# Optimization experiments

Hardware: AMD Instinct MI355X
Metric: run time of the kernel (lower is better)

The kernel has to match this reference:

```python
import jax, jax.numpy as jnp
import numpy as np
import math

VOCAB = 32000
D = 256
MAX_SEQ = 128
B, S = 32, 128
EPS = 1e-5


def cexp(p):
    # exp(1j*p) for real p, staying in complex64 under default x32
    return jax.lax.complex(jnp.cos(p), jnp.sin(p))


def setup_inputs() -> dict:
    key = jax.random.key(0)
    ks = jax.random.split(key, 10)
    x = jax.random.randint(ks[0], (B, S), 0, VOCAB)
    emb = jax.random.normal(ks[1], (VOCAB, D), dtype=jnp.float32)
    q_rot = jax.random.uniform(ks[2], (D,), minval=-math.pi, maxval=math.pi)
    k_rot = jax.random.uniform(ks[3], (D,), minval=-math.pi, maxval=math.pi)
    v_rot = jax.random.uniform(ks[4], (D,), minval=-math.pi, maxval=math.pi)
    # orthogonal init for ff_real via QR
    a = jax.random.normal(ks[5], (D, D), dtype=jnp.float32)
    q, r = jnp.linalg.qr(a)
    ff_real = q * jnp.sign(jnp.diag(r))[None, :]
    ff_imag = jax.random.uniform(ks[6], (D, D), minval=-0.01, maxval=0.01)
    wr = jax.random.normal(ks[7], (VOCAB, D), dtype=jnp.float32) / math.sqrt(D)
    br = jnp.zeros((VOCAB,), dtype=jnp.float32)
    wi = jax.random.normal(ks[8], (VOCAB, D), dtype=jnp.float32) / math.sqrt(D)
    bi = jnp.zeros((VOCAB,), dtype=jnp.float32)
    return {"x": x, "emb": emb, "q_rot": q_rot, "k_rot": k_rot, "v_rot": v_rot,
            "ff_real": ff_real, "ff_imag": ff_imag, "wr": wr, "br": br, "wi": wi, "bi": bi}


def _pos_phase(seq_len):
    pos = jnp.arange(MAX_SEQ, dtype=jnp.float32)[:, None]
    dim = jnp.arange(D, dtype=jnp.float32)[None, :]
    freq = 1.0 / (10000.0 ** (dim / D))
    return (pos * freq * math.pi)[:seq_len]  # [S, D]


def complex_norm(state):
    mag = jnp.abs(state)                                  # [B,S,D]
    mean_mag = mag.mean(axis=-1, keepdims=True)
    std_mag = jnp.std(mag, axis=-1, keepdims=True, ddof=1)  # torch default unbiased
    norm_mag = (mag - mean_mag) / (std_mag + EPS)
    scale = jnp.tanh(norm_mag) / (mag + EPS)
    return state * scale.astype(jnp.complex64)


def reference(x, emb, q_rot, k_rot, v_rot, ff_real, ff_imag, wr, br, wi, bi):
    seq_len = x.shape[1]
    mag = jnp.tanh(emb[x])                                # [B,S,D] float32
    state = mag.astype(jnp.complex64) * cexp(_pos_phase(seq_len))[None]  # [B,S,D] c64
    q = state * cexp(q_rot)
    k = state * cexp(k_rot)
    v = state * cexp(v_rot)
    interference = jnp.einsum('bsd,btd->bst', q, jnp.conj(k))
    attn_logits = interference.real / math.sqrt(D)        # [B,S,S]
    causal = jnp.tril(jnp.ones((seq_len, seq_len), dtype=bool))
    attn_logits = jnp.where(causal[None], attn_logits, -jnp.inf)
    attn_w = jax.nn.softmax(attn_logits * 8.0, axis=-1)   # [B,S,S]
    attn_out = jnp.einsum('bst,btd->bsd', attn_w.astype(jnp.complex64), v)
    state = state + attn_out
    ff = jax.lax.complex(ff_real, ff_imag)
    state = state @ ff                                    # [B,S,D]
    state = complex_norm(state)
    logits = state.real @ wr.T + br + state.imag @ wi.T + bi  # [B,S,V]
    return logits
```

## Files before the change

### kernel.cpp

```cpp
#include <hip/hip_runtime.h>

#define DD   256
#define SEQ  128
#define NB   32
#define VOC  32000
#define ROWS (NB * SEQ)
#define KK   512

typedef __attribute__((ext_vector_type(8))) short short8;
typedef __attribute__((ext_vector_type(4))) float f32x4;

__device__ inline unsigned short f2bf(float f) {
  unsigned int u = __float_as_uint(f);
  u += 0x7FFF + ((u >> 16) & 1);
  return (unsigned short)(u >> 16);
}

__device__ inline void gload16(const void* g, void* l) {
  __builtin_amdgcn_global_load_lds(
      (const __attribute__((address_space(1))) void*)g,
      (__attribute__((address_space(3))) void*)l, 16, 0, 0);
}

__global__ __launch_bounds__(256) void k_prep(
    const float* __restrict__ wr, const float* __restrict__ wi,
    const float* __restrict__ br, const float* __restrict__ bi,
    const float* __restrict__ qrot, const float* __restrict__ krot,
    const float* __restrict__ vrot,
    unsigned short* __restrict__ Wb, float* __restrict__ bias,
    float* __restrict__ rotcs) {
  int idx = blockIdx.x * 256 + threadIdx.x;
  int v = idx >> 7, c = idx & 127;
  const float* src = (c < 64) ? (wr + (size_t)v * DD + c * 4)
                              : (wi + (size_t)v * DD + (c - 64) * 4);
  float4 f = *(const float4*)src;
  ushort4 o;
  o.x = f2bf(f.x); o.y = f2bf(f.y); o.z = f2bf(f.z); o.w = f2bf(f.w);
  *(ushort4*)(Wb + (size_t)v * KK + c * 4) = o;
  if (c == 0) bias[v] = br[v] + bi[v];
  if (idx < DD) {
    float s0, c0;
    sincosf(qrot[idx], &s0, &c0); rotcs[idx] = c0;          rotcs[DD + idx] = s0;
    sincosf(krot[idx], &s0, &c0); rotcs[2 * DD + idx] = c0; rotcs[3 * DD + idx] = s0;
    sincosf(vrot[idx], &s0, &c0); rotcs[4 * DD + idx] = c0; rotcs[5 * DD + idx] = s0;
  }
}

__global__ __launch_bounds__(256) void k_embed(
    const int* __restrict__ x, const float* __restrict__ emb,
    const float* __restrict__ rotcs,
    float* __restrict__ Sb, float* __restrict__ Qb,
    float* __restrict__ Kb, float* __restrict__ Vb) {
  int row = blockIdx.x;
  int s = row & (SEQ - 1);
  int d = threadIdx.x;
  int tok = x[row];
  float m = tanhf(emb[(size_t)tok * DD + d]);
  float freq = __expf(-(float)d * (9.210340371976184f / 256.f));
  float p = (float)s * freq * 3.14159265358979f;
  float sp, cp;
  __sincosf(p, &sp, &cp);
  size_t base = (size_t)row * KK + d;
  Sb[base] = m * cp; Sb[base + DD] = m * sp;
  float cr, sr;
  cr = rotcs[d];          sr = rotcs[DD + d];
  Qb[base] = m * (cp * cr - sp * sr); Qb[base + DD] = m * (sp * cr + cp * sr);
  cr = rotcs[2 * DD + d]; sr = rotcs[3 * DD + d];
  Kb[base] = m * (cp * cr - sp * sr); Kb[base + DD] = m * (sp * cr + cp * sr);
  cr = rotcs[4 * DD + d]; sr = rotcs[5 * DD + d];
  Vb[base] = m * (cp * cr - sp * sr); Vb[base + DD] = m * (sp * cr + cp * sr);
}

#define QBLK 16
#define QPAD (KK + 4)
__global__ __launch_bounds__(512) void k_attn(
    const float* __restrict__ Qb, const float* __restrict__ Kb,
    const float* __restrict__ Vb, const float* __restrict__ Sb,
    float* __restrict__ S2) {
  int blk = blockIdx.x;
  int b = blk >> 3, g = blk & 7;
  int tid = threadIdx.x;
  int q = tid >> 5, t5 = tid & 31;
  int tt = t5 & 15, half = t5 >> 4;
  __shared__ __align__(16) float Ql[QBLK][QPAD];
  __shared__ __align__(16) float KVl[QBLK][QPAD];
  __shared__ float w[QBLK][SEQ];
  size_t qrow0 = (size_t)b * SEQ + g * QBLK;
  const float* qsrc = Qb + qrow0 * KK;
#pragma unroll
  for (int i = 0; i < 4; ++i) {
    int idx = i * 512 + tid;
    int r = idx >> 7, c = idx & 127;
    *(float4*)&Ql[r][c * 4] = *(const float4*)&qsrc[(size_t)r * KK + c * 4];
  }
  int ntile = g + 1;
  int srow = g * QBLK + q;
  for (int kt = 0; kt < ntile; ++kt) {
    __syncthreads();
    const float* ksrc = Kb + ((size_t)b * SEQ + kt * QBLK) * KK;
#pragma unroll
    for (int i = 0; i < 4; ++i) {
      int idx = i * 512 + tid;
      int r = idx >> 7, c = idx & 127;
      *(float4*)&KVl[r][c * 4] = *(const float4*)&ksrc[(size_t)r * KK + c * 4];
    }
    __syncthreads();
    const float4* qrow = (const float4*)&Ql[q][half * 256];
    const float4* krow = (const float4*)&KVl[tt][half * 256];
    float a0 = 0.f, a1 = 0.f, a2 = 0.f, a3 = 0.f;
#pragma unroll 8
    for (int cc = 0; cc < 64; ++cc) {
      float4 qa = qrow[cc], ka = krow[cc];
      a0 += qa.x * ka.x; a1 += qa.y * ka.y; a2 += qa.z * ka.z; a3 += qa.w * ka.w;
    }
    float acc = (a0 + a1) + (a2 + a3);
    acc += __shfl_xor(acc, 16);
    int t = kt * QBLK + tt;
    if (half == 0) w[q][t] = (t <= srow) ? acc * 0.5f : -INFINITY;
  }
  __syncthreads();
  int nk = ntile * QBLK;
  float mx = -INFINITY;
  for (int t = tt; t < nk; t += 16) mx = fmaxf(mx, w[q][t]);
#pragma unroll
  for (int o = 8; o; o >>= 1) mx = fmaxf(mx, __shfl_xor(mx, o));
  float sm = 0.f;
  for (int t = tt; t < nk; t += 16) {
    float e = __expf(w[q][t] - mx);
    if (half == 0) w[q][t] = e;
    sm += e;
  }
#pragma unroll
  for (int o = 8; o; o >>= 1) sm += __shfl_xor(sm, o);
  float inv = 1.f / sm;
  float4 facc[4] = {};
  for (int kt = 0; kt < ntile; ++kt) {
    __syncthreads();
    const float* vsrc = Vb + ((size_t)b * SEQ + kt * QBLK) * KK;
#pragma unroll
    for (int i = 0; i < 4; ++i) {
      int idx = i * 512 + tid;
      int r = idx >> 7, c = idx & 127;
      *(float4*)&KVl[r][c * 4] = *(const float4*)&vsrc[(size_t)r * KK + c * 4];
    }
    __syncthreads();
#pragma unroll
    for (int t1 = 0; t1 < QBLK; ++t1) {
      float wv = w[q][kt * QBLK + t1];
#pragma unroll
      for (int j = 0; j < 4; ++j) {
        float4 v4 = *(const float4*)&KVl[t1][tt * 4 + (j + 4 * half) * 64];
        facc[j].x += wv * v4.x; facc[j].y += wv * v4.y;
        facc[j].z += wv * v4.z; facc[j].w += wv * v4.w;
      }
    }
  }
  const float* ssrc = Sb + (qrow0 + q) * KK;
  float* dst = S2 + (qrow0 + q) * KK;
#pragma unroll
  for (int j = 0; j < 4; ++j) {
    int d0 = tt * 4 + (j + 4 * half) * 64;
    float4 sv = *(const float4*)&ssrc[d0];
    float4 o;
    o.x = sv.x + facc[j].x * inv; o.y = sv.y + facc[j].y * inv;
    o.z = sv.z + facc[j].z * inv; o.w = sv.w + facc[j].w * inv;
    *(float4*)&dst[d0] = o;
  }
}

__global__ __launch_bounds__(256) void k_ffnorm(
    const float* __restrict__ S2, const float* __restrict__ ffr,
    const float* __restrict__ ffi, unsigned short* __restrict__ X) {
  int row0 = blockIdx.x * 8;
  int d = threadIdx.x;
  __shared__ __align__(16) float in[8][KK];
  __shared__ float mg[8][DD];
  __shared__ float stats[16];
#pragma unroll
  for (int i = 0; i < 4; ++i) {
    int idx = i * 256 + d;
    *(float4*)&((float*)in)[idx * 4] = *(const float4*)&S2[(size_t)row0 * KK + idx * 4];
  }
  __syncthreads();
  float nr[8] = {0,0,0,0,0,0,0,0}, ni[8] = {0,0,0,0,0,0,0,0};
  for (int e4 = 0; e4 < 64; ++e4) {
    int e = e4 * 4;
    float fr0 = ffr[(e+0)*DD + d], fr1 = ffr[(e+1)*DD + d];
    float fr2 = ffr[(e+2)*DD + d], fr3 = ffr[(e+3)*DD + d];
    float fi0 = ffi[(e+0)*DD + d], fi1 = ffi[(e+1)*DD + d];
    float fi2 = ffi[(e+2)*DD + d], fi3 = ffi[(e+3)*DD + d];
#pragma unroll
    for (int r = 0; r < 8; ++r) {
      float4 av = *(const float4*)&in[r][e];
      float4 cv = *(const float4*)&in[r][DD + e];
      nr[r] += av.x*fr0 - cv.x*fi0 + av.y*fr1 - cv.y*fi1
             + av.z*fr2 - cv.z*fi2 + av.w*fr3 - cv.w*fi3;
      ni[r] += av.x*fi0 + cv.x*fr0 + av.y*fi1 + cv.y*fr1
             + av.z*fi2 + cv.z*fr2 + av.w*fi3 + cv.w*fr3;
    }
  }
#pragma unroll
  for (int r = 0; r < 8; ++r) mg[r][d] = sqrtf(nr[r]*nr[r] + ni[r]*ni[r]);
  __syncthreads();
  int wv = d >> 6, ln = d & 63;
#pragma unroll
  for (int k = 0; k < 2; ++k) {
    int r = wv + k * 4;
    float s0 = mg[r][ln] + mg[r][ln+64] + mg[r][ln+128] + mg[r][ln+192];
#pragma unroll
    for (int o = 32; o; o >>= 1) s0 += __shfl_xor(s0, o);
    float mean = s0 * (1.f / 256.f);
    float var = 0.f;
#pragma unroll
    for (int j = 0; j < 4; ++j) { float t2 = mg[r][ln + j*64] - mean; var += t2*t2; }
#pragma unroll
    for (int o = 32; o; o >>= 1) var += __shfl_xor(var, o);
    if (ln == 0) { stats[r*2] = mean; stats[r*2+1] = sqrtf(var * (1.f/255.f)); }
  }
  __syncthreads();
#pragma unroll
  for (int r = 0; r < 8; ++r) {
    float mean2 = stats[r*2], stdv = stats[r*2+1];
    float mag = mg[r][d];
    float norm = (mag - mean2) / (stdv + 1e-5f);
    float sc = tanhf(norm) / (mag + 1e-5f);
    size_t base = (size_t)(row0 + r) * KK + d;
    X[base] = f2bf(nr[r] * sc);
    X[base + DD] = f2bf(ni[r] * sc);
  }
}

__global__ __launch_bounds__(256, 3) void k_gemm(
    const unsigned short* __restrict__ X, const unsigned short* __restrict__ Wb,
    const float* __restrict__ bias, float* __restrict__ out) {
  __shared__ __align__(16) unsigned short At[128 * 64];
  __shared__ __align__(16) unsigned short Bt[128 * 64];
  int tid = threadIdx.x;
  int lane = tid & 63, wave = tid >> 6;
  int wr = wave >> 1, wc = wave & 1;
  int orig = blockIdx.x;
  int wg = (orig & 7) * 1000 + (orig >> 3);
  int mt = wg & 31, nt = wg >> 5;
  size_t rowA0 = (size_t)mt * 128;
  size_t rowB0 = (size_t)nt * 128;

  int srow = lane >> 3;
  int schunk = ((lane & 7) ^ (srow & 7)) * 8;

  f32x4 acc[4][4] = {};
  int l15 = lane & 15, hi = lane >> 4;

  for (int kt = 0; kt < 8; ++kt) {
    if (kt) { asm volatile("" ::: "memory"); __builtin_amdgcn_s_barrier(); }
    const int k0 = kt * 64;
#pragma unroll
    for (int j = 0; j < 4; ++j) {
      int rbase = wave * 32 + j * 8;
      gload16(&X [(rowA0 + rbase + srow) * KK + k0 + schunk], &At[rbase * 64]);
      gload16(&Wb[(rowB0 + rbase + srow) * KK + k0 + schunk], &Bt[rbase * 64]);
    }
    asm volatile("s_waitcnt vmcnt(0)" ::: "memory");
    __builtin_amdgcn_s_barrier();
    asm volatile("" ::: "memory");
#pragma unroll
    for (int ks = 0; ks < 2; ++ks) {
      int cXor = (ks * 4 + hi) ^ (l15 & 7);
      short8 a[4], bb[4];
#pragma unroll
      for (int ni = 0; ni < 4; ++ni)
        bb[ni] = *(const short8*)&Bt[(wc * 64 + ni * 16 + l15) * 64 + cXor * 8];
#pragma unroll
      for (int mi = 0; mi < 4; ++mi)
        a[mi] = *(const short8*)&At[(wr * 64 + mi * 16 + l15) * 64 + cXor * 8];
#pragma unroll
      for (int mi = 0; mi < 4; ++mi)
#pragma unroll
        for (int ni = 0; ni < 4; ++ni)
          acc[mi][ni] = __builtin_amdgcn_mfma_f32_16x16x32_bf16(a[mi], bb[ni], acc[mi][ni], 0, 0, 0);
    }
  }

  int cr = lane >> 4, cc = lane & 15;
#pragma unroll
  for (int ni = 0; ni < 4; ++ni) {
    size_t col = rowB0 + wc * 64 + ni * 16 + cc;
    float bv = bias[col];
#pragma unroll
    for (int mi = 0; mi < 4; ++mi) {
#pragma unroll
      for (int j = 0; j < 4; ++j) {
        size_t rowc = rowA0 + wr * 64 + mi * 16 + cr * 4 + j;
        __builtin_nontemporal_store(acc[mi][ni][j] + bv, &out[rowc * VOC + col]);
      }
    }
  }
}

extern "C" void kernel_launch(void* const* d_in, const int* in_sizes, int n_in,
                              void* d_out, int out_size, void* d_ws, size_t ws_size,
                              hipStream_t stream) {
  const int* x      = (const int*)d_in[0];
  const float* emb  = (const float*)d_in[1];
  const float* qrot = (const float*)d_in[2];
  const float* krot = (const float*)d_in[3];
  const float* vrot = (const float*)d_in[4];
  const float* ffr  = (const float*)d_in[5];
  const float* ffi  = (const float*)d_in[6];
  const float* wr   = (const float*)d_in[7];
  const float* br   = (const float*)d_in[8];
  const float* wi   = (const float*)d_in[9];
  const float* bi   = (const float*)d_in[10];
  float* out = (float*)d_out;
  char* ws = (char*)d_ws;

  unsigned short* Wb = (unsigned short*)ws;
  float* bias = (float*)(ws + 32768000);
  float* Sb = (float*)(ws + 32896000);
  float* Qb = Sb + (size_t)ROWS * KK;
  float* Kb = Qb + (size_t)ROWS * KK;
  float* Vb = Kb + (size_t)ROWS * KK;
  float* S2 = Vb + (size_t)ROWS * KK;
  unsigned short* Xb = (unsigned short*)(S2 + (size_t)ROWS * KK);
  float* rotcs = S2;

  k_prep<<<dim3(VOC * 128 / 256), dim3(256), 0, stream>>>(wr, wi, br, bi, qrot, krot, vrot, Wb, bias, rotcs);
  k_embed<<<dim3(ROWS), dim3(256), 0, stream>>>(x, emb, rotcs, Sb, Qb, Kb, Vb);
  k_attn<<<dim3(NB * 8), dim3(512), 0, stream>>>(Qb, Kb, Vb, Sb, S2);
  k_ffnorm<<<dim3(ROWS / 8), dim3(256), 0, stream>>>(S2, ffr, ffi, Xb);
  k_gemm<<<dim3(8000), dim3(256), 0, stream>>>(Xb, Wb, bias, out);
}
```

Measured before the change: 330.8 us.

## Double-buffer LDS tiles in the output GEMM to overlap loads with MFMA

The GEMM kernel now uses two LDS buffers for the A and B tiles. It prefetches the next K-slice through global_load_lds while MFMAs run on the current slice, with one barrier per iteration instead of a wait-then-barrier before compute. This aims to hide global-load latency behind compute. In exchange, LDS use doubles and the launch-bounds occupancy hint drops from 3 to 2 blocks per CU. That can reduce latency hiding across blocks in a kernel that is largely bound by output stores.

New measurement: 357.3 us. 8.0% more time.

```diff
diff --git a/kernel.cpp b/kernel.cpp
--- a/kernel.cpp
+++ b/kernel.cpp
@@ -230,11 +230,11 @@
   }
 }
 
-__global__ __launch_bounds__(256, 3) void k_gemm(
+__global__ __launch_bounds__(256, 2) void k_gemm(
     const unsigned short* __restrict__ X, const unsigned short* __restrict__ Wb,
     const float* __restrict__ bias, float* __restrict__ out) {
-  __shared__ __align__(16) unsigned short At[128 * 64];
-  __shared__ __align__(16) unsigned short Bt[128 * 64];
+  __shared__ __align__(16) unsigned short At[2][128 * 64];
+  __shared__ __align__(16) unsigned short Bt[2][128 * 64];
   int tid = threadIdx.x;
   int lane = tid & 63, wave = tid >> 6;
   int wr = wave >> 1, wc = wave & 1;
@@ -250,35 +250,41 @@
   f32x4 acc[4][4] = {};
   int l15 = lane & 15, hi = lane >> 4;
 
+#define STAGE(t, b)                                                         \
+  { const int k0 = (t) * 64;                                                \
+    _Pragma("unroll")                                                       \
+    for (int j = 0; j < 4; ++j) {                                           \
+      int rbase = wave * 32 + j * 8;                                        \
+      gload16(&X [(rowA0 + rbase + srow) * KK + k0 + schunk],               \
+              &At[b][rbase * 64]);                                          \
+      gload16(&Wb[(rowB0 + rbase + srow) * KK + k0 + schunk],               \
+              &Bt[b][rbase * 64]); } }
+
+  STAGE(0, 0);
+  __syncthreads();
+
   for (int kt = 0; kt < 8; ++kt) {
-    if (kt) { asm volatile("" ::: "memory"); __builtin_amdgcn_s_barrier(); }
-    const int k0 = kt * 64;
-#pragma unroll
-    for (int j = 0; j < 4; ++j) {
-      int rbase = wave * 32 + j * 8;
-      gload16(&X [(rowA0 + rbase + srow) * KK + k0 + schunk], &At[rbase * 64]);
-      gload16(&Wb[(rowB0 + rbase + srow) * KK + k0 + schunk], &Bt[rbase * 64]);
-    }
-    asm volatile("s_waitcnt vmcnt(0)" ::: "memory");
-    __builtin_amdgcn_s_barrier();
-    asm volatile("" ::: "memory");
+    int buf = kt & 1;
+    if (kt < 7) STAGE(kt + 1, buf ^ 1);
 #pragma unroll
     for (int ks = 0; ks < 2; ++ks) {
       int cXor = (ks * 4 + hi) ^ (l15 & 7);
       short8 a[4], bb[4];
 #pragma unroll
       for (int ni = 0; ni < 4; ++ni)
-        bb[ni] = *(const short8*)&Bt[(wc * 64 + ni * 16 + l15) * 64 + cXor * 8];
+        bb[ni] = *(const short8*)&Bt[buf][(wc * 64 + ni * 16 + l15) * 64 + cXor * 8];
 #pragma unroll
       for (int mi = 0; mi < 4; ++mi)
-        a[mi] = *(const short8*)&At[(wr * 64 + mi * 16 + l15) * 64 + cXor * 8];
+        a[mi] = *(const short8*)&At[buf][(wr * 64 + mi * 16 + l15) * 64 + cXor * 8];
 #pragma unroll
       for (int mi = 0; mi < 4; ++mi)
 #pragma unroll
         for (int ni = 0; ni < 4; ++ni)
           acc[mi][ni] = __builtin_amdgcn_mfma_f32_16x16x32_bf16(a[mi], bb[ni], acc[mi][ni], 0, 0, 0);
     }
-  }
+    __syncthreads();
+  }
+#undef STAGE
 
   int cr = lane >> 4, cc = lane & 15;
 #pragma unroll
```

## Fold weight bf16 conversion into attention launch and compute rotations inline

Applied to the files above, without the earlier changes.

Removes the separate prep kernel. The weight-to-bf16 conversion and bias sum now run as extra blocks appended to the attention kernel grid, so that bandwidth-bound work can overlap with the small 256-block attention launch. The q/k/v rotation sin/cos values are computed per thread inside the embed kernel instead of being read from a precomputed table. The output GEMM also switches from nontemporal stores to plain stores. Trade-offs: each conversion block now asks for the attention kernel's LDS and 512-thread resources, embed threads do redundant sincosf work, and plain stores may pollute the cache.

Result: slower. 376.2 us (+13.7%).

```diff
diff --git a/kernel.cpp b/kernel.cpp
--- a/kernel.cpp
+++ b/kernel.cpp
@@ -22,33 +22,10 @@
       (__attribute__((address_space(3))) void*)l, 16, 0, 0);
 }
 
-__global__ __launch_bounds__(256) void k_prep(
-    const float* __restrict__ wr, const float* __restrict__ wi,
-    const float* __restrict__ br, const float* __restrict__ bi,
+__global__ __launch_bounds__(256) void k_embed(
+    const int* __restrict__ x, const float* __restrict__ emb,
     const float* __restrict__ qrot, const float* __restrict__ krot,
     const float* __restrict__ vrot,
-    unsigned short* __restrict__ Wb, float* __restrict__ bias,
-    float* __restrict__ rotcs) {
-  int idx = blockIdx.x * 256 + threadIdx.x;
-  int v = idx >> 7, c = idx & 127;
-  const float* src = (c < 64) ? (wr + (size_t)v * DD + c * 4)
-                              : (wi + (size_t)v * DD + (c - 64) * 4);
-  float4 f = *(const float4*)src;
-  ushort4 o;
-  o.x = f2bf(f.x); o.y = f2bf(f.y); o.z = f2bf(f.z); o.w = f2bf(f.w);
-  *(ushort4*)(Wb + (size_t)v * KK + c * 4) = o;
-  if (c == 0) bias[v] = br[v] + bi[v];
-  if (idx < DD) {
-    float s0, c0;
-    sincosf(qrot[idx], &s0, &c0); rotcs[idx] = c0;          rotcs[DD + idx] = s0;
-    sincosf(krot[idx], &s0, &c0); rotcs[2 * DD + idx] = c0; rotcs[3 * DD + idx] = s0;
-    sincosf(vrot[idx], &s0, &c0); rotcs[4 * DD + idx] = c0; rotcs[5 * DD + idx] = s0;
-  }
-}
-
-__global__ __launch_bounds__(256) void k_embed(
-    const int* __restrict__ x, const float* __restrict__ emb,
-    const float* __restrict__ rotcs,
     float* __restrict__ Sb, float* __restrict__ Qb,
     float* __restrict__ Kb, float* __restrict__ Vb) {
   int row = blockIdx.x;
@@ -63,23 +40,38 @@
   size_t base = (size_t)row * KK + d;
   Sb[base] = m * cp; Sb[base + DD] = m * sp;
   float cr, sr;
-  cr = rotcs[d];          sr = rotcs[DD + d];
+  sincosf(qrot[d], &sr, &cr);
   Qb[base] = m * (cp * cr - sp * sr); Qb[base + DD] = m * (sp * cr + cp * sr);
-  cr = rotcs[2 * DD + d]; sr = rotcs[3 * DD + d];
+  sincosf(krot[d], &sr, &cr);
   Kb[base] = m * (cp * cr - sp * sr); Kb[base + DD] = m * (sp * cr + cp * sr);
-  cr = rotcs[4 * DD + d]; sr = rotcs[5 * DD + d];
+  sincosf(vrot[d], &sr, &cr);
   Vb[base] = m * (cp * cr - sp * sr); Vb[base + DD] = m * (sp * cr + cp * sr);
 }
 
 #define QBLK 16
 #define QPAD (KK + 4)
-__global__ __launch_bounds__(512) void k_attn(
+__global__ __launch_bounds__(512) void k_attn_prep(
     const float* __restrict__ Qb, const float* __restrict__ Kb,
     const float* __restrict__ Vb, const float* __restrict__ Sb,
-    float* __restrict__ S2) {
+    float* __restrict__ S2,
+    const float* __restrict__ wr, const float* __restrict__ wi,
+    const float* __restrict__ br, const float* __restrict__ bi,
+    unsigned short* __restrict__ Wb, float* __restrict__ bias) {
+  int tid = threadIdx.x;
+  if (blockIdx.x >= 256) {
+    int idx = (blockIdx.x - 256) * 512 + tid;
+    int v = idx >> 7, c = idx & 127;
+    const float* src = (c < 64) ? (wr + (size_t)v * DD + c * 4)
+                                : (wi + (size_t)v * DD + (c - 64) * 4);
+    float4 f = *(const float4*)src;
+    ushort4 o;
+    o.x = f2bf(f.x); o.y = f2bf(f.y); o.z = f2bf(f.z); o.w = f2bf(f.w);
+    *(ushort4*)(Wb + (size_t)v * KK + c * 4) = o;
+    if (c == 0) bias[v] = br[v] + bi[v];
+    return;
+  }
   int blk = blockIdx.x;
   int b = blk >> 3, g = blk & 7;
-  int tid = threadIdx.x;
   int q = tid >> 5, t5 = tid & 31;
   int tt = t5 & 15, half = t5 >> 4;
   __shared__ __align__(16) float Ql[QBLK][QPAD];
@@ -290,7 +282,7 @@
 #pragma unroll
       for (int j = 0; j < 4; ++j) {
         size_t rowc = rowA0 + wr * 64 + mi * 16 + cr * 4 + j;
-        __builtin_nontemporal_store(acc[mi][ni][j] + bv, &out[rowc * VOC + col]);
+        out[rowc * VOC + col] = acc[mi][ni][j] + bv;
       }
     }
   }
@@ -321,11 +313,10 @@
   float* Vb = Kb + (size_t)ROWS * KK;
   float* S2 = Vb + (size_t)ROWS * KK;
   unsigned short* Xb = (unsigned short*)(S2 + (size_t)ROWS * KK);
-  float* rotcs = S2;
-
-  k_prep<<<dim3(VOC * 128 / 256), dim3(256), 0, stream>>>(wr, wi, br, bi, qrot, krot, vrot, Wb, bias, rotcs);
-  k_embed<<<dim3(ROWS), dim3(256), 0, stream>>>(x, emb, rotcs, Sb, Qb, Kb, Vb);
-  k_attn<<<dim3(NB * 8), dim3(512), 0, stream>>>(Qb, Kb, Vb, Sb, S2);
+
+  k_embed<<<dim3(ROWS), dim3(256), 0, stream>>>(x, emb, qrot, krot, vrot, Sb, Qb, Kb, Vb);
+  k_attn_prep<<<dim3(256 + 8000), dim3(512), 0, stream>>>(Qb, Kb, Vb, Sb, S2,
+                                                          wr, wi, br, bi, Wb, bias);
   k_ffnorm<<<dim3(ROWS / 8), dim3(256), 0, stream>>>(S2, ffr, ffi, Xb);
   k_gemm<<<dim3(8000), dim3(256), 0, stream>>>(Xb, Wb, bias, out);
 }
```
